# Kernel tuning notes

Measured on AMD Instinct MI355X. Metric: run time of the kernel, lower is better.

## Reference

```python
import jax, jax.numpy as jnp
import numpy as np

N = 50000
E = 800000
IN_C = 256
OUT_C = 128
HID = 2 * OUT_C


def gcn_conv(x, edge_index, W, b):
    """PyG GCNConv: add self-loops, symmetric deg normalization, linear, scatter-add."""
    n = x.shape[0]
    row, col = edge_index[0], edge_index[1]
    loops = jnp.arange(n, dtype=edge_index.dtype)
    row = jnp.concatenate([row, loops])  # source nodes
    col = jnp.concatenate([col, loops])  # target nodes
    deg = jax.ops.segment_sum(jnp.ones(row.shape[0], dtype=x.dtype), col, num_segments=n)
    dinv = jnp.where(deg > 0, jax.lax.rsqrt(deg), 0.0)
    norm = dinv[row] * dinv[col]  # [E+N]
    h = x @ W  # [n, out]
    msg = norm[:, None] * h[row]  # gather + scale
    return jax.ops.segment_sum(msg, col, num_segments=n) + b


def setup_inputs() -> dict:
    key = jax.random.key(0)
    ks = jax.random.split(key, 16)
    inp = {}
    for i in range(4):
        inp[f"x{i+1}"] = jax.random.normal(ks[i], (N, IN_C), dtype=jnp.float32)
        inp[f"edge_index{i+1}"] = jax.random.randint(ks[4 + i], (2, E), 0, N, dtype=jnp.int32)
    s_in = 1.0 / np.sqrt(IN_C)
    s_hid = 1.0 / np.sqrt(HID)
    inp["Wc"] = jax.random.uniform(ks[8], (4, IN_C, HID), jnp.float32, -s_in, s_in)
    inp["bc"] = jnp.zeros((4, HID), jnp.float32)
    inp["Wm"] = jax.random.uniform(ks[9], (4, HID, OUT_C), jnp.float32, -s_hid, s_hid)
    inp["bm"] = jnp.zeros((4, OUT_C), jnp.float32)
    inp["Wl"] = jax.random.uniform(ks[10], (4, HID, OUT_C), jnp.float32, -s_hid, s_hid)
    inp["bl"] = jnp.zeros((4, OUT_C), jnp.float32)
    return inp


def reference(x1, edge_index1, x2, edge_index2, x3, edge_index3, x4, edge_index4,
              Wc, bc, Wm, bm, Wl, bl):
    xs = [x1, x2, x3, x4]
    eis = [edge_index1, edge_index2, edge_index3, edge_index4]
    mus, logstds = [], []
    for i in range(4):
        h = gcn_conv(xs[i], eis[i], Wc[i], bc[i])
        mus.append(gcn_conv(h, eis[i], Wm[i], bm[i]))
        logstds.append(gcn_conv(h, eis[i], Wl[i], bl[i]))
    return (jnp.stack(mus), jnp.stack(logstds))  # each [4, N, OUT_C]
```

## Files before the change

kernel.cpp:

```cpp
#include <hip/hip_runtime.h>

#define NN 50000
#define NE 800000

typedef __attribute__((ext_vector_type(8))) short short8;
typedef __attribute__((ext_vector_type(4))) short short4v;
typedef __attribute__((ext_vector_type(4))) unsigned short ushort4v;
typedef __attribute__((ext_vector_type(4))) float floatx4;

__device__ inline unsigned short bf16_hi_trunc(float x) {
    return (unsigned short)(__builtin_bit_cast(unsigned, x) >> 16);
}
__device__ inline unsigned short bf16_lo_rne(float x) {
    unsigned hu = __builtin_bit_cast(unsigned, x) & 0xFFFF0000u;
    float rest = x - __builtin_bit_cast(float, hu);
    unsigned r = __builtin_bit_cast(unsigned, rest);
    r += 0x7FFFu + ((r >> 16) & 1u);
    return (unsigned short)(r >> 16);
}
__device__ inline unsigned short bf16_rne(float x) {
    unsigned r = __builtin_bit_cast(unsigned, x);
    r += 0x7FFFu + ((r >> 16) & 1u);
    return (unsigned short)(r >> 16);
}
__device__ inline float bfu_to_f(unsigned short u) {
    return __builtin_bit_cast(float, ((unsigned)u) << 16);
}
__device__ inline floatx4 bf4_to_f4(ushort4v v) {
    floatx4 r;
    r[0] = bfu_to_f(v[0]); r[1] = bfu_to_f(v[1]);
    r[2] = bfu_to_f(v[2]); r[3] = bfu_to_f(v[3]);
    return r;
}

__global__ void count_all_kernel(const int* __restrict__ c0, const int* __restrict__ c1,
                                 const int* __restrict__ c2, const int* __restrict__ c3,
                                 int* __restrict__ cnt, int E, int N) {
    int e = blockIdx.x * blockDim.x + threadIdx.x;
    if (e >= E) return;
    int g = blockIdx.y;
    const int* col = (g == 0) ? c0 : (g == 1) ? c1 : (g == 2) ? c2 : c3;
    atomicAdd(&cnt[(size_t)g * N + col[e]], 1);
}

__global__ __launch_bounds__(1024) void scan_dinv_kernel(const int* __restrict__ cnt_all,
                                                         int* __restrict__ offs_all,
                                                         float* __restrict__ dinv_all, int N) {
    __shared__ int sums[1024];
    const int T = 1024;
    int g = blockIdx.x;
    const int* cnt = cnt_all + (size_t)g * N;
    int* offs = offs_all + (size_t)g * (N + 1);
    float* dinv = dinv_all + (size_t)g * N;

    int tid = threadIdx.x;
    int chunk = (N + T - 1) / T;
    int start = tid * chunk;
    int end = start + chunk; if (end > N) end = N;
    int s = 0;
    for (int i = start; i < end; ++i) s += cnt[i];
    sums[tid] = s;
    __syncthreads();
    for (int off = 1; off < T; off <<= 1) {
        int v = (tid >= off) ? sums[tid - off] : 0;
        __syncthreads();
        sums[tid] += v;
        __syncthreads();
    }
    int run = sums[tid] - s;
    for (int i = start; i < end; ++i) {
        offs[i] = run;
        int c = cnt[i];
        run += c;
        dinv[i] = rsqrtf((float)(c + 1));
    }
    if (tid == T - 1) offs[N] = sums[T - 1];
}

__global__ void fill_all_kernel(const int* __restrict__ ei0, const int* __restrict__ ei1,
                                const int* __restrict__ ei2, const int* __restrict__ ei3,
                                const int* __restrict__ offs, int* __restrict__ cursor,
                                const float* __restrict__ dinv,
                                int2* __restrict__ rec, int E, int N) {
    int e = blockIdx.x * blockDim.x + threadIdx.x;
    if (e >= E) return;
    int g = blockIdx.y;
    const int* ei = (g == 0) ? ei0 : (g == 1) ? ei1 : (g == 2) ? ei2 : ei3;
    int r = ei[e], c = ei[E + e];
    int p = atomicAdd(&cursor[(size_t)g * N + c], 1);
    int idx = offs[(size_t)g * (N + 1) + c] + p;
    int2 v;
    v.x = r;
    v.y = __builtin_bit_cast(int, dinv[(size_t)g * N + r] * dinv[(size_t)g * N + c]);
    rec[(size_t)g * E + idx] = v;
}

__global__ __launch_bounds__(256) void pack_w_kernel(const float* __restrict__ Wc,
                                                     const float* __restrict__ Wm,
                                                     const float* __restrict__ Wl,
                                                     short* __restrict__ WcT_hi,
                                                     short* __restrict__ WcT_lo,
                                                     short* __restrict__ WmlT_hi,
                                                     short* __restrict__ WmlT_lo) {
    int idx = blockIdx.x * 256 + threadIdx.x;
    int g = idx >> 16;
    int n = (idx >> 8) & 255;
    int k = idx & 255;
    float wc = Wc[((size_t)(g * 256 + k) * 256) + n];
    WcT_hi[idx] = (short)bf16_hi_trunc(wc);
    WcT_lo[idx] = (short)bf16_lo_rne(wc);
    float wml = (n < 128) ? Wm[((size_t)(g * 256 + k) * 128) + n]
                          : Wl[((size_t)(g * 256 + k) * 128) + (n - 128)];
    WmlT_hi[idx] = (short)bf16_hi_trunc(wml);
    WmlT_lo[idx] = (short)bf16_lo_rne(wml);
}

template <bool BF16_OUT>
__global__ __launch_bounds__(256) void gemm_mfma_kernel(const float* __restrict__ A,
                                                        const short* __restrict__ Bt_hi,
                                                        const short* __restrict__ Bt_lo,
                                                        void* __restrict__ Cout, int M, int Nc) {
    __shared__ __align__(16) short As_hi[128][40];
    __shared__ __align__(16) short As_lo[128][40];

    int t = threadIdx.x;
    int lane = t & 63;
    int wave = t >> 6;
    int wm = (wave & 1) * 64;
    int wn = (wave >> 1) * 64;
    int row_blk = blockIdx.y * 128;
    int col_blk = blockIdx.x * 128;

    int kq = (t & 7) * 4;
    int rb = t >> 3;

    int al = lane & 15;
    int ak = (lane >> 4) * 8;

    floatx4 acc[4][4] = {};

    for (int k0 = 0; k0 < 256; k0 += 32) {
        __syncthreads();
#pragma unroll
        for (int p = 0; p < 4; ++p) {
            int r = rb + p * 32;
            int gr = row_blk + r;
            float4 v = make_float4(0.f, 0.f, 0.f, 0.f);
            if (gr < M) v = *(const float4*)(A + (size_t)gr * 256 + k0 + kq);
            short4v h4, l4;
            h4[0] = (short)bf16_hi_trunc(v.x); l4[0] = (short)bf16_lo_rne(v.x);
            h4[1] = (short)bf16_hi_trunc(v.y); l4[1] = (short)bf16_lo_rne(v.y);
            h4[2] = (short)bf16_hi_trunc(v.z); l4[2] = (short)bf16_lo_rne(v.z);
            h4[3] = (short)bf16_hi_trunc(v.w); l4[3] = (short)bf16_lo_rne(v.w);
            *(short4v*)&As_hi[r][kq] = h4;
            *(short4v*)&As_lo[r][kq] = l4;
        }
        __syncthreads();

        short8 bh[4], bl4[4];
#pragma unroll
        for (int nt = 0; nt < 4; ++nt) {
            const short* ph = Bt_hi + (size_t)(col_blk + wn + nt * 16 + al) * 256 + k0 + ak;
            const short* pl = Bt_lo + (size_t)(col_blk + wn + nt * 16 + al) * 256 + k0 + ak;
            bh[nt] = *(const short8*)ph;
            bl4[nt] = *(const short8*)pl;
        }

#pragma unroll
        for (int mt = 0; mt < 4; ++mt) {
            short8 ah = *(const short8*)&As_hi[wm + mt * 16 + al][ak];
            short8 alo = *(const short8*)&As_lo[wm + mt * 16 + al][ak];
#pragma unroll
            for (int nt = 0; nt < 4; ++nt) {
                acc[mt][nt] = __builtin_amdgcn_mfma_f32_16x16x32_bf16(ah, bh[nt], acc[mt][nt], 0, 0, 0);
                acc[mt][nt] = __builtin_amdgcn_mfma_f32_16x16x32_bf16(ah, bl4[nt], acc[mt][nt], 0, 0, 0);
                acc[mt][nt] = __builtin_amdgcn_mfma_f32_16x16x32_bf16(alo, bh[nt], acc[mt][nt], 0, 0, 0);
            }
        }
    }

    int rq = lane >> 4;
#pragma unroll
    for (int mt = 0; mt < 4; ++mt) {
        int rbase = row_blk + wm + mt * 16 + rq * 4;
#pragma unroll
        for (int reg = 0; reg < 4; ++reg) {
            int r = rbase + reg;
            if (r < M) {
#pragma unroll
                for (int nt = 0; nt < 4; ++nt) {
                    size_t ci = (size_t)r * Nc + col_blk + wn + nt * 16 + al;
                    if constexpr (BF16_OUT) {
                        ((unsigned short*)Cout)[ci] = bf16_rne(acc[mt][nt][reg]);
                    } else {
                        ((float*)Cout)[ci] = acc[mt][nt][reg];
                    }
                }
            }
        }
    }
}

__global__ __launch_bounds__(256) void agg_bf16_kernel(const unsigned short* __restrict__ Hlin,
                                                       const float* __restrict__ dinv,
                                                       const int* __restrict__ offs,
                                                       const int2* __restrict__ rec,
                                                       const float* __restrict__ bias,
                                                       float* __restrict__ Hout) {
    int node = __builtin_amdgcn_readfirstlane(blockIdx.x * 4 + (threadIdx.x >> 6));
    if (node >= NN) return;
    int lane = threadIdx.x & 63;

    float di = dinv[node];
    float dd = di * di;
    floatx4 acc = *(const floatx4*)(bias + 4 * lane);
    floatx4 self = bf4_to_f4(*(const ushort4v*)(Hlin + (size_t)node * 256 + 4 * lane));
    acc += dd * self;

    int s = __builtin_amdgcn_readfirstlane(offs[node]);
    int e = __builtin_amdgcn_readfirstlane(offs[node + 1]);
    int j = s;
    for (; j + 4 <= e; j += 4) {
        int2 r0 = rec[j + 0], r1 = rec[j + 1], r2 = rec[j + 2], r3 = rec[j + 3];
        floatx4 v0 = bf4_to_f4(*(const ushort4v*)(Hlin + (size_t)r0.x * 256 + 4 * lane));
        floatx4 v1 = bf4_to_f4(*(const ushort4v*)(Hlin + (size_t)r1.x * 256 + 4 * lane));
        floatx4 v2 = bf4_to_f4(*(const ushort4v*)(Hlin + (size_t)r2.x * 256 + 4 * lane));
        floatx4 v3 = bf4_to_f4(*(const ushort4v*)(Hlin + (size_t)r3.x * 256 + 4 * lane));
        acc += __builtin_bit_cast(float, r0.y) * v0;
        acc += __builtin_bit_cast(float, r1.y) * v1;
        acc += __builtin_bit_cast(float, r2.y) * v2;
        acc += __builtin_bit_cast(float, r3.y) * v3;
    }
    for (; j < e; ++j) {
        int2 r0 = rec[j];
        floatx4 v0 = bf4_to_f4(*(const ushort4v*)(Hlin + (size_t)r0.x * 256 + 4 * lane));
        acc += __builtin_bit_cast(float, r0.y) * v0;
    }
    *(floatx4*)(Hout + (size_t)node * 256 + 4 * lane) = acc;
}

__global__ __launch_bounds__(256) void agg_dual_kernel(const float* __restrict__ Lin,
                                                       const float* __restrict__ dinv,
                                                       const int* __restrict__ offs,
                                                       const int2* __restrict__ rec,
                                                       const float* __restrict__ bm,
                                                       const float* __restrict__ bl,
                                                       float* __restrict__ out_mu,
                                                       float* __restrict__ out_ls) {
    int node = __builtin_amdgcn_readfirstlane(blockIdx.x * 4 + (threadIdx.x >> 6));
    if (node >= NN) return;
    int lane = threadIdx.x & 63;

    float di = dinv[node];
    float dd = di * di;
    const float* bp = (lane < 32) ? (bm + 4 * lane) : (bl + 4 * (lane - 32));
    floatx4 acc = *(const floatx4*)bp;
    floatx4 self = *(const floatx4*)(Lin + (size_t)node * 256 + 4 * lane);
    acc += dd * self;

    int s = __builtin_amdgcn_readfirstlane(offs[node]);
    int e = __builtin_amdgcn_readfirstlane(offs[node + 1]);
    int j = s;
    for (; j + 4 <= e; j += 4) {
        int2 r0 = rec[j + 0], r1 = rec[j + 1], r2 = rec[j + 2], r3 = rec[j + 3];
        floatx4 v0 = *(const floatx4*)(Lin + (size_t)r0.x * 256 + 4 * lane);
        floatx4 v1 = *(const floatx4*)(Lin + (size_t)r1.x * 256 + 4 * lane);
        floatx4 v2 = *(const floatx4*)(Lin + (size_t)r2.x * 256 + 4 * lane);
        floatx4 v3 = *(const floatx4*)(Lin + (size_t)r3.x * 256 + 4 * lane);
        acc += __builtin_bit_cast(float, r0.y) * v0;
        acc += __builtin_bit_cast(float, r1.y) * v1;
        acc += __builtin_bit_cast(float, r2.y) * v2;
        acc += __builtin_bit_cast(float, r3.y) * v3;
    }
    for (; j < e; ++j) {
        int2 r0 = rec[j];
        floatx4 v0 = *(const floatx4*)(Lin + (size_t)r0.x * 256 + 4 * lane);
        acc += __builtin_bit_cast(float, r0.y) * v0;
    }
    float* op = (lane < 32) ? (out_mu + (size_t)node * 128 + 4 * lane)
                            : (out_ls + (size_t)node * 128 + 4 * (lane - 32));
    *(floatx4*)op = acc;
}

extern "C" void kernel_launch(void* const* d_in, const int* in_sizes, int n_in,
                              void* d_out, int out_size, void* d_ws, size_t ws_size,
                              hipStream_t stream) {
    const int N = NN, E = NE;
    const float* Wc = (const float*)d_in[8];
    const float* bc = (const float*)d_in[9];
    const float* Wm = (const float*)d_in[10];
    const float* bm = (const float*)d_in[11];
    const float* Wl = (const float*)d_in[12];
    const float* bl = (const float*)d_in[13];
    float* out = (float*)d_out;

    float* buf_lin  = (float*)d_ws;
    float* buf_h    = buf_lin + (size_t)N * 256;
    float* dinv     = buf_h + (size_t)N * 256;
    int*   cnt      = (int*)(dinv + 4 * (size_t)N);
    int*   offs     = cnt + 4 * (size_t)N;
    int*   cursor   = offs + 4 * ((size_t)N + 1);
    int2*  csr_rec  = (int2*)(cursor + 4 * (size_t)N);
    short* WcT_hi   = (short*)(csr_rec + 4 * (size_t)E);
    short* WcT_lo   = WcT_hi + 4 * 65536;
    short* WmlT_hi  = WcT_lo + 4 * 65536;
    short* WmlT_lo  = WmlT_hi + 4 * 65536;

    const int* ei0 = (const int*)d_in[1];
    const int* ei1 = (const int*)d_in[3];
    const int* ei2 = (const int*)d_in[5];
    const int* ei3 = (const int*)d_in[7];

    pack_w_kernel<<<1024, 256, 0, stream>>>(Wc, Wm, Wl, WcT_hi, WcT_lo, WmlT_hi, WmlT_lo);
    hipMemsetAsync(cnt, 0, 4 * (size_t)N * sizeof(int), stream);
    hipMemsetAsync(cursor, 0, 4 * (size_t)N * sizeof(int), stream);
    count_all_kernel<<<dim3((E + 255) / 256, 4), 256, 0, stream>>>(
        ei0 + E, ei1 + E, ei2 + E, ei3 + E, cnt, E, N);
    scan_dinv_kernel<<<4, 1024, 0, stream>>>(cnt, offs, dinv, N);
    fill_all_kernel<<<dim3((E + 255) / 256, 4), 256, 0, stream>>>(
        ei0, ei1, ei2, ei3, offs, cursor, dinv, csr_rec, E, N);

    for (int g = 0; g < 4; ++g) {
        const float* x = (const float*)d_in[2 * g];
        const float* dv = dinv + (size_t)g * N;
        const int* of = offs + (size_t)g * (N + 1);
        const int2* cr = csr_rec + (size_t)g * E;

        gemm_mfma_kernel<true><<<dim3(2, (N + 127) / 128), 256, 0, stream>>>(
            x, WcT_hi + (size_t)g * 65536, WcT_lo + (size_t)g * 65536, buf_lin, N, 256);
        agg_bf16_kernel<<<(N + 3) / 4, 256, 0, stream>>>(
            (const unsigned short*)buf_lin, dv, of, cr, bc + (size_t)g * 256, buf_h);
        gemm_mfma_kernel<false><<<dim3(2, (N + 127) / 128), 256, 0, stream>>>(
            buf_h, WmlT_hi + (size_t)g * 65536, WmlT_lo + (size_t)g * 65536, buf_lin, N, 256);
        agg_dual_kernel<<<(N + 3) / 4, 256, 0, stream>>>(
            buf_lin, dv, of, cr, bm + (size_t)g * 128, bl + (size_t)g * 128,
            out + (size_t)g * N * 128, out + (size_t)(4 + g) * N * 128);
    }
}
```

Before: 1.951 ms.

## Split bf16 aggregation edges across half-waves with 16-byte gathers, deepen dual unroll

The bf16 aggregation kernel now has each half-wave handle alternating edges, with each lane loading 8 bf16 values (16 bytes) per gather. The two halves' partial sums are combined with a cross-lane shuffle, which gives twice as many independent gathers in flight per wave. The fp32 dual aggregation loop is unrolled from 4 to 8 edges to expose more memory-level parallelism. The CSR fill seeds the cursor with prefix offsets during the scan, dropping a memset and an offs load in the fill. The cost is more registers and a shuffle-reduction step.

```diff
diff --git a/kernel.cpp b/kernel.cpp
--- a/kernel.cpp
+++ b/kernel.cpp
@@ -6,6 +6,7 @@
 typedef __attribute__((ext_vector_type(8))) short short8;
 typedef __attribute__((ext_vector_type(4))) short short4v;
 typedef __attribute__((ext_vector_type(4))) unsigned short ushort4v;
+typedef __attribute__((ext_vector_type(8))) unsigned short ushort8v;
 typedef __attribute__((ext_vector_type(4))) float floatx4;
 
 __device__ inline unsigned short bf16_hi_trunc(float x) {
@@ -25,12 +26,6 @@
 }
 __device__ inline float bfu_to_f(unsigned short u) {
     return __builtin_bit_cast(float, ((unsigned)u) << 16);
-}
-__device__ inline floatx4 bf4_to_f4(ushort4v v) {
-    floatx4 r;
-    r[0] = bfu_to_f(v[0]); r[1] = bfu_to_f(v[1]);
-    r[2] = bfu_to_f(v[2]); r[3] = bfu_to_f(v[3]);
-    return r;
 }
 
 __global__ void count_all_kernel(const int* __restrict__ c0, const int* __restrict__ c1,
@@ -45,12 +40,14 @@
 
 __global__ __launch_bounds__(1024) void scan_dinv_kernel(const int* __restrict__ cnt_all,
                                                          int* __restrict__ offs_all,
+                                                         int* __restrict__ cursor_all,
                                                          float* __restrict__ dinv_all, int N) {
     __shared__ int sums[1024];
     const int T = 1024;
     int g = blockIdx.x;
     const int* cnt = cnt_all + (size_t)g * N;
     int* offs = offs_all + (size_t)g * (N + 1);
+    int* cursor = cursor_all + (size_t)g * N;
     float* dinv = dinv_all + (size_t)g * N;
 
     int tid = threadIdx.x;
@@ -70,6 +67,7 @@
     int run = sums[tid] - s;
     for (int i = start; i < end; ++i) {
         offs[i] = run;
+        cursor[i] = run;
         int c = cnt[i];
         run += c;
         dinv[i] = rsqrtf((float)(c + 1));
@@ -79,7 +77,7 @@
 
 __global__ void fill_all_kernel(const int* __restrict__ ei0, const int* __restrict__ ei1,
                                 const int* __restrict__ ei2, const int* __restrict__ ei3,
-                                const int* __restrict__ offs, int* __restrict__ cursor,
+                                int* __restrict__ cursor,
                                 const float* __restrict__ dinv,
                                 int2* __restrict__ rec, int E, int N) {
     int e = blockIdx.x * blockDim.x + threadIdx.x;
@@ -87,8 +85,7 @@
     int g = blockIdx.y;
     const int* ei = (g == 0) ? ei0 : (g == 1) ? ei1 : (g == 2) ? ei2 : ei3;
     int r = ei[e], c = ei[E + e];
-    int p = atomicAdd(&cursor[(size_t)g * N + c], 1);
-    int idx = offs[(size_t)g * (N + 1) + c] + p;
+    int idx = atomicAdd(&cursor[(size_t)g * N + c], 1);
     int2 v;
     v.x = r;
     v.y = __builtin_bit_cast(int, dinv[(size_t)g * N + r] * dinv[(size_t)g * N + c]);
@@ -210,33 +207,63 @@
     int node = __builtin_amdgcn_readfirstlane(blockIdx.x * 4 + (threadIdx.x >> 6));
     if (node >= NN) return;
     int lane = threadIdx.x & 63;
+    int half = lane >> 5;
+    int colb = (lane & 31) * 8;
 
     float di = dinv[node];
     float dd = di * di;
-    floatx4 acc = *(const floatx4*)(bias + 4 * lane);
-    floatx4 self = bf4_to_f4(*(const ushort4v*)(Hlin + (size_t)node * 256 + 4 * lane));
-    acc += dd * self;
-
     int s = __builtin_amdgcn_readfirstlane(offs[node]);
     int e = __builtin_amdgcn_readfirstlane(offs[node + 1]);
-    int j = s;
-    for (; j + 4 <= e; j += 4) {
-        int2 r0 = rec[j + 0], r1 = rec[j + 1], r2 = rec[j + 2], r3 = rec[j + 3];
-        floatx4 v0 = bf4_to_f4(*(const ushort4v*)(Hlin + (size_t)r0.x * 256 + 4 * lane));
-        floatx4 v1 = bf4_to_f4(*(const ushort4v*)(Hlin + (size_t)r1.x * 256 + 4 * lane));
-        floatx4 v2 = bf4_to_f4(*(const ushort4v*)(Hlin + (size_t)r2.x * 256 + 4 * lane));
-        floatx4 v3 = bf4_to_f4(*(const ushort4v*)(Hlin + (size_t)r3.x * 256 + 4 * lane));
-        acc += __builtin_bit_cast(float, r0.y) * v0;
-        acc += __builtin_bit_cast(float, r1.y) * v1;
-        acc += __builtin_bit_cast(float, r2.y) * v2;
-        acc += __builtin_bit_cast(float, r3.y) * v3;
-    }
-    for (; j < e; ++j) {
+
+    float accv[8];
+    {
+        ushort8v sv = *(const ushort8v*)(Hlin + (size_t)node * 256 + colb);
+        floatx4 b0 = *(const floatx4*)(bias + colb);
+        floatx4 b1 = *(const floatx4*)(bias + colb + 4);
+        float hsel = (half == 0) ? 1.f : 0.f;
+#pragma unroll
+        for (int i = 0; i < 4; ++i) accv[i] = hsel * (b0[i] + dd * bfu_to_f(sv[i]));
+#pragma unroll
+        for (int i = 0; i < 4; ++i) accv[4 + i] = hsel * (b1[i] + dd * bfu_to_f(sv[4 + i]));
+    }
+
+    int j = s + half;
+    for (; j + 6 < e; j += 8) {
+        int2 r0 = rec[j + 0], r1 = rec[j + 2], r2 = rec[j + 4], r3 = rec[j + 6];
+        ushort8v v0 = *(const ushort8v*)(Hlin + (size_t)r0.x * 256 + colb);
+        ushort8v v1 = *(const ushort8v*)(Hlin + (size_t)r1.x * 256 + colb);
+        ushort8v v2 = *(const ushort8v*)(Hlin + (size_t)r2.x * 256 + colb);
+        ushort8v v3 = *(const ushort8v*)(Hlin + (size_t)r3.x * 256 + colb);
+        float n0 = __builtin_bit_cast(float, r0.y);
+        float n1 = __builtin_bit_cast(float, r1.y);
+        float n2 = __builtin_bit_cast(float, r2.y);
+        float n3 = __builtin_bit_cast(float, r3.y);
+#pragma unroll
+        for (int i = 0; i < 8; ++i) {
+            accv[i] += n0 * bfu_to_f(v0[i]);
+            accv[i] += n1 * bfu_to_f(v1[i]);
+            accv[i] += n2 * bfu_to_f(v2[i]);
+            accv[i] += n3 * bfu_to_f(v3[i]);
+        }
+    }
+    for (; j < e; j += 2) {
         int2 r0 = rec[j];
-        floatx4 v0 = bf4_to_f4(*(const ushort4v*)(Hlin + (size_t)r0.x * 256 + 4 * lane));
-        acc += __builtin_bit_cast(float, r0.y) * v0;
-    }
-    *(floatx4*)(Hout + (size_t)node * 256 + 4 * lane) = acc;
+        ushort8v v0 = *(const ushort8v*)(Hlin + (size_t)r0.x * 256 + colb);
+        float n0 = __builtin_bit_cast(float, r0.y);
+#pragma unroll
+        for (int i = 0; i < 8; ++i) accv[i] += n0 * bfu_to_f(v0[i]);
+    }
+
+#pragma unroll
+    for (int i = 0; i < 8; ++i) accv[i] += __shfl_xor(accv[i], 32);
+
+    if (lane < 32) {
+        floatx4 o0, o1;
+#pragma unroll
+        for (int i = 0; i < 4; ++i) { o0[i] = accv[i]; o1[i] = accv[4 + i]; }
+        *(floatx4*)(Hout + (size_t)node * 256 + colb) = o0;
+        *(floatx4*)(Hout + (size_t)node * 256 + colb + 4) = o1;
+    }
 }
 
 __global__ __launch_bounds__(256) void agg_dual_kernel(const float* __restrict__ Lin,
@@ -261,16 +288,25 @@
     int s = __builtin_amdgcn_readfirstlane(offs[node]);
     int e = __builtin_amdgcn_readfirstlane(offs[node + 1]);
     int j = s;
-    for (; j + 4 <= e; j += 4) {
+    for (; j + 8 <= e; j += 8) {
         int2 r0 = rec[j + 0], r1 = rec[j + 1], r2 = rec[j + 2], r3 = rec[j + 3];
+        int2 r4 = rec[j + 4], r5 = rec[j + 5], r6 = rec[j + 6], r7 = rec[j + 7];
         floatx4 v0 = *(const floatx4*)(Lin + (size_t)r0.x * 256 + 4 * lane);
         floatx4 v1 = *(const floatx4*)(Lin + (size_t)r1.x * 256 + 4 * lane);
         floatx4 v2 = *(const floatx4*)(Lin + (size_t)r2.x * 256 + 4 * lane);
         floatx4 v3 = *(const floatx4*)(Lin + (size_t)r3.x * 256 + 4 * lane);
+        floatx4 v4 = *(const floatx4*)(Lin + (size_t)r4.x * 256 + 4 * lane);
+        floatx4 v5 = *(const floatx4*)(Lin + (size_t)r5.x * 256 + 4 * lane);
+        floatx4 v6 = *(const floatx4*)(Lin + (size_t)r6.x * 256 + 4 * lane);
+        floatx4 v7 = *(const floatx4*)(Lin + (size_t)r7.x * 256 + 4 * lane);
         acc += __builtin_bit_cast(float, r0.y) * v0;
         acc += __builtin_bit_cast(float, r1.y) * v1;
         acc += __builtin_bit_cast(float, r2.y) * v2;
         acc += __builtin_bit_cast(float, r3.y) * v3;
+        acc += __builtin_bit_cast(float, r4.y) * v4;
+        acc += __builtin_bit_cast(float, r5.y) * v5;
+        acc += __builtin_bit_cast(float, r6.y) * v6;
+        acc += __builtin_bit_cast(float, r7.y) * v7;
     }
     for (; j < e; ++j) {
         int2 r0 = rec[j];
@@ -313,12 +349,11 @@
 
     pack_w_kernel<<<1024, 256, 0, stream>>>(Wc, Wm, Wl, WcT_hi, WcT_lo, WmlT_hi, WmlT_lo);
     hipMemsetAsync(cnt, 0, 4 * (size_t)N * sizeof(int), stream);
-    hipMemsetAsync(cursor, 0, 4 * (size_t)N * sizeof(int), stream);
     count_all_kernel<<<dim3((E + 255) / 256, 4), 256, 0, stream>>>(
         ei0 + E, ei1 + E, ei2 + E, ei3 + E, cnt, E, N);
-    scan_dinv_kernel<<<4, 1024, 0, stream>>>(cnt, offs, dinv, N);
+    scan_dinv_kernel<<<4, 1024, 0, stream>>>(cnt, offs, cursor, dinv, N);
     fill_all_kernel<<<dim3((E + 255) / 256, 4), 256, 0, stream>>>(
-        ei0, ei1, ei2, ei3, offs, cursor, dinv, csr_rec, E, N);
+        ei0, ei1, ei2, ei3, cursor, dinv, csr_rec, E, N);
 
     for (int g = 0; g < 4; ++g) {
         const float* x = (const float*)d_in[2 * g];
```

New measurement: 1.974 ms. No clear change (+1.2%).

## Build CSR via bucketed binning with shared-memory cursors instead of global atomics

Applied to the files above, without the earlier changes.

The count pass now also drops each edge into one of 196 buckets of 256 destination nodes, packing the source and the local destination into a single 32-bit word. A new fill kernel then takes one bucket per block, keeps that bucket's per-node cursors and dinv values in shared memory, and scatters the CSR records using LDS atomics. This replaces the global per-node cursor atomics and fully random record writes with writes that stay inside a narrow CSR region, and removes one memset. In exchange it adds a staging pass through the reused buf_lin workspace. It assumes no bucket holds more than 6144 edges and that source ids fit in 16 bits, so a skewed degree distribution would silently drop edges.

```diff
diff --git a/kernel.cpp b/kernel.cpp
--- a/kernel.cpp
+++ b/kernel.cpp
@@ -2,6 +2,8 @@
 
 #define NN 50000
 #define NE 800000
+#define NBUCK 196
+#define BCAP 6144
 
 typedef __attribute__((ext_vector_type(8))) short short8;
 typedef __attribute__((ext_vector_type(4))) short short4v;
@@ -33,14 +35,22 @@
     return r;
 }
 
-__global__ void count_all_kernel(const int* __restrict__ c0, const int* __restrict__ c1,
-                                 const int* __restrict__ c2, const int* __restrict__ c3,
-                                 int* __restrict__ cnt, int E, int N) {
+__global__ void bin_count_kernel(const int* __restrict__ ei0, const int* __restrict__ ei1,
+                                 const int* __restrict__ ei2, const int* __restrict__ ei3,
+                                 int* __restrict__ cnt, int* __restrict__ bcur,
+                                 unsigned* __restrict__ bin, int E, int N) {
     int e = blockIdx.x * blockDim.x + threadIdx.x;
     if (e >= E) return;
     int g = blockIdx.y;
-    const int* col = (g == 0) ? c0 : (g == 1) ? c1 : (g == 2) ? c2 : c3;
-    atomicAdd(&cnt[(size_t)g * N + col[e]], 1);
+    const int* ei = (g == 0) ? ei0 : (g == 1) ? ei1 : (g == 2) ? ei2 : ei3;
+    int src = ei[e];
+    int dst = ei[E + e];
+    atomicAdd(&cnt[(size_t)g * N + dst], 1);
+    int b = dst >> 8;
+    int idx = atomicAdd(&bcur[g * 256 + b], 1);
+    if (idx < BCAP)
+        bin[((size_t)(g * NBUCK + b)) * BCAP + idx] =
+            (unsigned)src | ((unsigned)(dst & 255) << 16);
 }
 
 __global__ __launch_bounds__(1024) void scan_dinv_kernel(const int* __restrict__ cnt_all,
@@ -77,22 +87,39 @@
     if (tid == T - 1) offs[N] = sums[T - 1];
 }
 
-__global__ void fill_all_kernel(const int* __restrict__ ei0, const int* __restrict__ ei1,
-                                const int* __restrict__ ei2, const int* __restrict__ ei3,
-                                const int* __restrict__ offs, int* __restrict__ cursor,
-                                const float* __restrict__ dinv,
-                                int2* __restrict__ rec, int E, int N) {
-    int e = blockIdx.x * blockDim.x + threadIdx.x;
-    if (e >= E) return;
+__global__ __launch_bounds__(256) void fill2_kernel(const unsigned* __restrict__ bin,
+                                                    const int* __restrict__ offs_all,
+                                                    const float* __restrict__ dinv_all,
+                                                    int2* __restrict__ rec_all, int E, int N) {
+    int b = blockIdx.x;
     int g = blockIdx.y;
-    const int* ei = (g == 0) ? ei0 : (g == 1) ? ei1 : (g == 2) ? ei2 : ei3;
-    int r = ei[e], c = ei[E + e];
-    int p = atomicAdd(&cursor[(size_t)g * N + c], 1);
-    int idx = offs[(size_t)g * (N + 1) + c] + p;
-    int2 v;
-    v.x = r;
-    v.y = __builtin_bit_cast(int, dinv[(size_t)g * N + r] * dinv[(size_t)g * N + c]);
-    rec[(size_t)g * E + idx] = v;
+    const int* offs = offs_all + (size_t)g * (N + 1);
+    const float* dinv = dinv_all + (size_t)g * N;
+    int2* rec = rec_all + (size_t)g * E;
+
+    __shared__ int lcur[256];
+    __shared__ float ldv[256];
+    int t = threadIdx.x;
+    int node0 = b * 256;
+    int nn = N - node0; if (nn > 256) nn = 256;
+    if (t < nn) {
+        lcur[t] = offs[node0 + t];
+        ldv[t] = dinv[node0 + t];
+    }
+    __syncthreads();
+
+    int nb = offs[node0 + nn] - offs[node0];
+    const unsigned* bb = bin + ((size_t)(g * NBUCK + b)) * BCAP;
+    for (int i = t; i < nb; i += 256) {
+        unsigned u = bb[i];
+        int src = (int)(u & 0xFFFFu);
+        int dl = (int)((u >> 16) & 255u);
+        int pos = atomicAdd(&lcur[dl], 1);
+        int2 v;
+        v.x = src;
+        v.y = __builtin_bit_cast(int, ldv[dl] * dinv[src]);
+        rec[pos] = v;
+    }
 }
 
 __global__ __launch_bounds__(256) void pack_w_kernel(const float* __restrict__ Wc,
@@ -294,17 +321,18 @@
     const float* bl = (const float*)d_in[13];
     float* out = (float*)d_out;
 
-    float* buf_lin  = (float*)d_ws;
-    float* buf_h    = buf_lin + (size_t)N * 256;
-    float* dinv     = buf_h + (size_t)N * 256;
-    int*   cnt      = (int*)(dinv + 4 * (size_t)N);
-    int*   offs     = cnt + 4 * (size_t)N;
-    int*   cursor   = offs + 4 * ((size_t)N + 1);
-    int2*  csr_rec  = (int2*)(cursor + 4 * (size_t)N);
-    short* WcT_hi   = (short*)(csr_rec + 4 * (size_t)E);
-    short* WcT_lo   = WcT_hi + 4 * 65536;
-    short* WmlT_hi  = WcT_lo + 4 * 65536;
-    short* WmlT_lo  = WmlT_hi + 4 * 65536;
+    float*    buf_lin = (float*)d_ws;
+    float*    buf_h   = buf_lin + (size_t)N * 256;
+    float*    dinv    = buf_h + (size_t)N * 256;
+    int*      cnt     = (int*)(dinv + 4 * (size_t)N);
+    int*      bcur    = cnt + 4 * (size_t)N;
+    int*      offs    = bcur + 4 * 256;
+    int2*     csr_rec = (int2*)(offs + 4 * ((size_t)N + 1));
+    short*    WcT_hi  = (short*)(csr_rec + 4 * (size_t)E);
+    short*    WcT_lo  = WcT_hi + 4 * 65536;
+    short*    WmlT_hi = WcT_lo + 4 * 65536;
+    short*    WmlT_lo = WmlT_hi + 4 * 65536;
+    unsigned* bin     = (unsigned*)buf_lin;
 
     const int* ei0 = (const int*)d_in[1];
     const int* ei1 = (const int*)d_in[3];
@@ -312,13 +340,11 @@
     const int* ei3 = (const int*)d_in[7];
 
     pack_w_kernel<<<1024, 256, 0, stream>>>(Wc, Wm, Wl, WcT_hi, WcT_lo, WmlT_hi, WmlT_lo);
-    hipMemsetAsync(cnt, 0, 4 * (size_t)N * sizeof(int), stream);
-    hipMemsetAsync(cursor, 0, 4 * (size_t)N * sizeof(int), stream);
-    count_all_kernel<<<dim3((E + 255) / 256, 4), 256, 0, stream>>>(
-        ei0 + E, ei1 + E, ei2 + E, ei3 + E, cnt, E, N);
+    hipMemsetAsync(cnt, 0, (4 * (size_t)N + 4 * 256) * sizeof(int), stream);
+    bin_count_kernel<<<dim3((E + 255) / 256, 4), 256, 0, stream>>>(
+        ei0, ei1, ei2, ei3, cnt, bcur, bin, E, N);
     scan_dinv_kernel<<<4, 1024, 0, stream>>>(cnt, offs, dinv, N);
-    fill_all_kernel<<<dim3((E + 255) / 256, 4), 256, 0, stream>>>(
-        ei0, ei1, ei2, ei3, offs, cursor, dinv, csr_rec, E, N);
+    fill2_kernel<<<dim3(NBUCK, 4), 256, 0, stream>>>(bin, offs, dinv, csr_rec, E, N);
 
     for (int g = 0; g < 4; ++g) {
         const float* x = (const float*)d_in[2 * g];
```

Result: slower. 3.131 ms (+60.5%).
